# Kernel tuning notes

Hardware: AMD Instinct MI355X
Metric: run time of the kernel (lower is better)

## Reference

```python
import jax, jax.numpy as jnp
import numpy as np

MAX_SPIKE_TIME = 100.0
TH = 1.0
BIT = 8
K = 3
PAD = 1
OUT_CH = 64


def _unfold3x3(x):
    # torch F.unfold(kernel=3, padding=1, stride=1): output (B, C*9, H*W),
    # feature order channel-major then (kh, kw).
    B, C, H, W = x.shape
    xp = jnp.pad(x, ((0, 0), (0, 0), (PAD, PAD), (PAD, PAD)))
    cols = [xp[:, :, i:i + H, j:j + W] for i in range(K) for j in range(K)]
    p = jnp.stack(cols, axis=2)            # (B, C, 9, H, W)
    return p.reshape(B, C * K * K, H * W)  # (B, C*9, L)


def _weight_quantization(w):
    # tanh -> scale by global abs-max (no grad through alpha) -> round with STE
    w = jnp.tanh(w)
    alpha = jax.lax.stop_gradient(jnp.max(jnp.abs(w)))
    qmax = float(2 ** (BIT - 1) - 1)
    w = jnp.clip(w / alpha, -1.0, 1.0) * qmax
    w_hat = jax.lax.stop_gradient(jnp.round(w) - w) + w
    return w_hat * alpha / qmax


def _t_linear_c(patches, weight):
    # patches: (B, L, F_in); weight: (F_out, F_in)
    sorted_inp = jnp.sort(patches, axis=-1)      # (B, L, F_in)
    indic = jnp.argsort(patches, axis=-1)        # (B, L, F_in)
    wT = weight.T                                # (F_in, F_out)
    w_sorted = wT[indic]                         # (B, L, F_in, F_out)
    wq = _weight_quantization(w_sorted)
    si = sorted_inp[..., None]                   # (B, L, F_in, 1)
    weight_input_mul = si * wq
    weight_sum = jnp.cumsum(wq, axis=-2)
    input_weight_sum = jnp.cumsum(weight_input_mul, axis=-2)
    out_all = input_weight_sum / jnp.clip(weight_sum - TH, 1e-10, 1e10)
    out_spike = jnp.where(weight_sum < TH, MAX_SPIKE_TIME, out_all)
    out_spike = jnp.where(out_spike < si, MAX_SPIKE_TIME, out_spike)
    # causality check against the NEXT sorted input time (1.0 for the last slot)
    next_in = jnp.concatenate([si[..., 1:, :], jnp.ones_like(si[..., :1, :])], axis=-2)
    out_spike = jnp.where(out_spike > next_in, MAX_SPIKE_TIME, out_spike)
    return jnp.min(out_spike, axis=-2)           # (B, L, F_out)


def setup_inputs() -> dict:
    key = jax.random.key(0)
    k1, k2 = jax.random.split(key)
    inp = jax.random.uniform(k1, (4, 16, 32, 32), dtype=jnp.float32)
    in_features = K * K * 16
    weight = jax.random.uniform(k2, (OUT_CH, in_features), dtype=jnp.float32) * (10.0 / in_features)
    return {"inp": inp, "weight": weight}


def reference(inp, weight):
    B, C, H, W = inp.shape
    patches = _unfold3x3(inp).transpose(0, 2, 1)          # (B, L, F_in)
    patches = jnp.where(patches < 0.1, MAX_SPIKE_TIME, patches)
    out = _t_linear_c(patches, weight)                    # (B, L, F_out)
    out = out.transpose(0, 2, 1).reshape(B, OUT_CH, H, W)  # stride=1, pad=1 -> same HW
    return out
```

## Files before the change

### kernel.cpp

```cpp
#include <hip/hip_runtime.h>
#include <math.h>

constexpr int F_IN   = 144;
constexpr int F_OUT  = 64;
constexpr int H_IMG  = 32;
constexpr int W_IMG  = 32;
constexpr int NPIX   = 4 * H_IMG * W_IMG;
#define MAX_SPIKE 100.0f

__global__ __launch_bounds__(256) void quant_fused_kernel(
    const float* __restrict__ w,
    float* __restrict__ wqT)
{
#pragma clang fp contract(off)
    __shared__ float wred[4];
    const int tid = threadIdx.x;

    float m = 0.f;
    for (int i = tid; i < F_OUT * F_IN; i += 256)
        m = fmaxf(m, fabsf(w[i]));
    for (int s = 32; s > 0; s >>= 1)
        m = fmaxf(m, __shfl_xor(m, s, 64));
    if ((tid & 63) == 0) wred[tid >> 6] = m;
    __syncthreads();
    const float mw = fmaxf(fmaxf(wred[0], wred[1]), fmaxf(wred[2], wred[3]));
    const float alpha = (float)::tanh((double)mw);

    const int i = blockIdx.x * 256 + tid;
    const int o = i / F_IN;
    const int f = i - o * F_IN;
    const float t = (float)::tanh((double)w[i]);
    float x = t / alpha;
    x = fminf(fmaxf(x, -1.f), 1.f) * 127.f;
    const float r = rintf(x);
    wqT[f * F_OUT + o] = r * alpha / 127.f;
}

__global__ __launch_bounds__(256) void spike_conv_kernel(
    const float* __restrict__ inp,
    const float* __restrict__ wq,
    float* __restrict__ out)
{
#pragma clang fp contract(off)
    __shared__ unsigned long long kr[4][F_IN];
    __shared__ float sv[4][F_IN + 1];

    const int tid  = threadIdx.x;
    const int lane = tid & 63;
    const int wv_i = tid >> 6;
    const int p    = blockIdx.x * 4 + wv_i;
    const int b    = p >> 10;
    const int l    = p & 1023;
    const int h    = l >> 5;
    const int w    = l & 31;

    float v0f, v1f, v2f;
    unsigned long long key0, key1, key2;
    {
        int idx[3] = { lane, lane + 64, lane + 128 };
        float vals[3];
        for (int m = 0; m < 3; ++m) {
            const int i = idx[m];
            float v = MAX_SPIKE;
            if (i < F_IN) {
                const int c  = i / 9;
                const int r  = i - c * 9;
                const int kh = r / 3;
                const int kw = r - kh * 3;
                const int hh = h + kh - 1;
                const int ww = w + kw - 1;
                float x = 0.f;
                if (hh >= 0 && hh < H_IMG && ww >= 0 && ww < W_IMG)
                    x = inp[((b * 16 + c) * H_IMG + hh) * W_IMG + ww];
                v = (x < 0.1f) ? MAX_SPIKE : x;
                kr[wv_i][i] = ((unsigned long long)__float_as_uint(v) << 8)
                              | (unsigned)i;
            }
            vals[m] = v;
        }
        v0f = vals[0]; v1f = vals[1]; v2f = vals[2];
        key0 = ((unsigned long long)__float_as_uint(v0f) << 8) | (unsigned)idx[0];
        key1 = ((unsigned long long)__float_as_uint(v1f) << 8) | (unsigned)idx[1];
        key2 = ((unsigned long long)__float_as_uint(v2f) << 8) | (unsigned)idx[2];
        if (lane == 0) sv[wv_i][F_IN] = 1.0f;
    }
    __syncthreads();

    int r0 = 0, r1 = 0, r2 = 0;
    {
        const unsigned long long* ks = kr[wv_i];
#pragma unroll 4
        for (int j = 0; j < F_IN; ++j) {
            const unsigned long long kj = ks[j];
            r0 += (kj < key0);
            r1 += (kj < key1);
            r2 += (kj < key2);
        }
    }
    __syncthreads();

    {
        unsigned* krlo = (unsigned*)&kr[wv_i][0];
        sv[wv_i][r0] = v0f;  krlo[2 * r0] = (unsigned)lane << 8;
        sv[wv_i][r1] = v1f;  krlo[2 * r1] = (unsigned)(lane + 64) << 8;
        if (lane < F_IN - 128) {
            sv[wv_i][r2] = v2f;  krlo[2 * r2] = (unsigned)(lane + 128) << 8;
        }
    }
    __syncthreads();

    {
        unsigned* krhi = (unsigned*)&kr[wv_i][0];
        for (int k = lane; k < F_IN; k += 64)
            krhi[2 * k + 1] = __float_as_uint(sv[wv_i][k + 1]);
    }
    __syncthreads();

    const char* wqp = (const char*)(wq + lane);
    float s   = sv[wv_i][0];
    float ws  = 0.f;
    float iws = 0.f;
    float mn  = MAX_SPIKE;
    bool  done = false;
    for (int k = 0; k < F_IN; ++k) {
        if (s >= MAX_SPIKE) break;
        const unsigned long long rec = kr[wv_i][k];
        const float nxt = __uint_as_float((unsigned)(rec >> 32));
        const float wvv = *(const float*)(wqp + (unsigned)rec);
        ws += wvv;
        const float prod = s * wvv;
        iws += prod;
        if (!__all(ws < 1.0f)) {
            float d = fmaxf(ws - 1.0f, 1e-10f);
            const float q = iws / d;
            const bool valid = (ws >= 1.0f) && (q >= s) && (q <= nxt);
            if (valid && !done) { mn = q; done = true; }
            if (__all(done)) break;
        }
        s = nxt;
    }
    out[(b * F_OUT + lane) * 1024 + l] = mn;
}

extern "C" void kernel_launch(void* const* d_in, const int* in_sizes, int n_in,
                              void* d_out, int out_size, void* d_ws, size_t ws_size,
                              hipStream_t stream) {
    const float* inp = (const float*)d_in[0];
    const float* w   = (const float*)d_in[1];
    float* out = (float*)d_out;
    float* wqT = (float*)d_ws;

    quant_fused_kernel<<<36, 256, 0, stream>>>(w, wqT);
    spike_conv_kernel<<<NPIX / 4, 256, 0, stream>>>(inp, wqT, out);
}
```

Measured before the change: 100.1 us.

## Stage quantized weights in LDS, batch 8 pixels per block, unroll scan by 8

Each block now copies the full 144x64 quantized weight table (36 KB) into LDS and handles 8 pixels (512 threads) instead of 4. Weight lookups in the spike scan come from LDS instead of global memory. The rank computation reads keys in pairs, and the sequential scan is unrolled in groups of 8 so the wave-wide threshold check runs once per group. This cuts global gather latency and branch overhead, but adds a per-block weight copy, more LDS pressure that may limit occupancy, and up to 7 extra iterations of work past the early exit.

```diff
diff --git a/kernel.cpp b/kernel.cpp
--- a/kernel.cpp
+++ b/kernel.cpp
@@ -6,6 +6,8 @@
 constexpr int H_IMG  = 32;
 constexpr int W_IMG  = 32;
 constexpr int NPIX   = 4 * H_IMG * W_IMG;
+constexpr int PPB    = 8;
+constexpr int NTHR   = PPB * 64;
 #define MAX_SPIKE 100.0f
 
 __global__ __launch_bounds__(256) void quant_fused_kernel(
@@ -36,23 +38,31 @@
     wqT[f * F_OUT + o] = r * alpha / 127.f;
 }
 
-__global__ __launch_bounds__(256) void spike_conv_kernel(
+__global__ __launch_bounds__(NTHR, 4) void spike_conv_kernel(
     const float* __restrict__ inp,
     const float* __restrict__ wq,
     float* __restrict__ out)
 {
 #pragma clang fp contract(off)
-    __shared__ unsigned long long kr[4][F_IN];
-    __shared__ float sv[4][F_IN + 1];
+    __shared__ __align__(16) float wql[F_IN * F_OUT];
+    __shared__ __align__(16) unsigned long long kr[PPB][F_IN];
+    __shared__ float sv[PPB][F_IN + 1];
 
     const int tid  = threadIdx.x;
     const int lane = tid & 63;
     const int wv_i = tid >> 6;
-    const int p    = blockIdx.x * 4 + wv_i;
+    const int p    = blockIdx.x * PPB + wv_i;
     const int b    = p >> 10;
     const int l    = p & 1023;
     const int h    = l >> 5;
     const int w    = l & 31;
+
+    {
+        const float4* src = (const float4*)wq;
+        float4* dst = (float4*)wql;
+        for (int i = tid; i < (F_IN * F_OUT) / 4; i += NTHR)
+            dst[i] = src[i];
+    }
 
     float v0f, v1f, v2f;
     unsigned long long key0, key1, key2;
@@ -88,23 +98,23 @@
 
     int r0 = 0, r1 = 0, r2 = 0;
     {
-        const unsigned long long* ks = kr[wv_i];
+        const ulonglong2* ks2 = (const ulonglong2*)&kr[wv_i][0];
 #pragma unroll 4
-        for (int j = 0; j < F_IN; ++j) {
-            const unsigned long long kj = ks[j];
-            r0 += (kj < key0);
-            r1 += (kj < key1);
-            r2 += (kj < key2);
+        for (int j = 0; j < F_IN / 2; ++j) {
+            const ulonglong2 kk = ks2[j];
+            r0 += (kk.x < key0) + (kk.y < key0);
+            r1 += (kk.x < key1) + (kk.y < key1);
+            r2 += (kk.x < key2) + (kk.y < key2);
         }
     }
     __syncthreads();
 
     {
         unsigned* krlo = (unsigned*)&kr[wv_i][0];
-        sv[wv_i][r0] = v0f;  krlo[2 * r0] = (unsigned)lane << 8;
-        sv[wv_i][r1] = v1f;  krlo[2 * r1] = (unsigned)(lane + 64) << 8;
+        sv[wv_i][r0] = v0f;  krlo[2 * r0] = (unsigned)lane << 6;
+        sv[wv_i][r1] = v1f;  krlo[2 * r1] = (unsigned)(lane + 64) << 6;
         if (lane < F_IN - 128) {
-            sv[wv_i][r2] = v2f;  krlo[2 * r2] = (unsigned)(lane + 128) << 8;
+            sv[wv_i][r2] = v2f;  krlo[2 * r2] = (unsigned)(lane + 128) << 6;
         }
     }
     __syncthreads();
@@ -116,28 +126,43 @@
     }
     __syncthreads();
 
-    const char* wqp = (const char*)(wq + lane);
     float s   = sv[wv_i][0];
     float ws  = 0.f;
     float iws = 0.f;
     float mn  = MAX_SPIKE;
     bool  done = false;
-    for (int k = 0; k < F_IN; ++k) {
+    const ulonglong2* rec2 = (const ulonglong2*)&kr[wv_i][0];
+    for (int k0 = 0; k0 < F_IN; k0 += 8) {
         if (s >= MAX_SPIKE) break;
-        const unsigned long long rec = kr[wv_i][k];
-        const float nxt = __uint_as_float((unsigned)(rec >> 32));
-        const float wvv = *(const float*)(wqp + (unsigned)rec);
-        ws += wvv;
-        const float prod = s * wvv;
-        iws += prod;
-        if (!__all(ws < 1.0f)) {
-            float d = fmaxf(ws - 1.0f, 1e-10f);
-            const float q = iws / d;
-            const bool valid = (ws >= 1.0f) && (q >= s) && (q <= nxt);
-            if (valid && !done) { mn = q; done = true; }
+        const ulonglong2 ra = rec2[(k0 >> 1) + 0];
+        const ulonglong2 rb = rec2[(k0 >> 1) + 1];
+        const ulonglong2 rc = rec2[(k0 >> 1) + 2];
+        const ulonglong2 rd = rec2[(k0 >> 1) + 3];
+        const unsigned long long r8[8] = { ra.x, ra.y, rb.x, rb.y,
+                                           rc.x, rc.y, rd.x, rd.y };
+        float su[8], nx[8], wsu[8], iwsu[8];
+#pragma unroll
+        for (int u = 0; u < 8; ++u) {
+            su[u] = s;
+            nx[u] = __uint_as_float((unsigned)(r8[u] >> 32));
+            const float wvv = wql[(unsigned)r8[u] + lane];
+            ws += wvv;
+            const float prod = su[u] * wvv;
+            iws += prod;
+            wsu[u]  = ws;
+            iwsu[u] = iws;
+            s = nx[u];
+        }
+        if (!__all(wsu[7] < 1.0f)) {
+#pragma unroll
+            for (int u = 0; u < 8; ++u) {
+                const float d = fmaxf(wsu[u] - 1.0f, 1e-10f);
+                const float q = iwsu[u] / d;
+                const bool valid = (wsu[u] >= 1.0f) & (q >= su[u]) & (q <= nx[u]);
+                if (valid & !done) { mn = q; done = true; }
+            }
             if (__all(done)) break;
         }
-        s = nxt;
     }
     out[(b * F_OUT + lane) * 1024 + l] = mn;
 }
@@ -151,5 +176,5 @@
     float* wqT = (float*)d_ws;
 
     quant_fused_kernel<<<36, 256, 0, stream>>>(w, wqT);
-    spike_conv_kernel<<<NPIX / 4, 256, 0, stream>>>(inp, wqT, out);
+    spike_conv_kernel<<<NPIX / PPB, NTHR, 0, stream>>>(inp, wqT, out);
 }
```

Result: faster. 84.54 us (-15.5%).
